# Kernel tuning notes

Measured on AMD Instinct MI355X. Metric: run time of the kernel, lower is better.

## Reference

```python
import jax, jax.numpy as jnp
import numpy as np

N = 50000   # nodes
E = 800000  # edges
F = 64      # node_feature_dim
H = 128     # hidden_dim


def setup_inputs() -> dict:
    key = jax.random.key(0)
    ks = jax.random.split(key, 20)
    def w(k, shape, fan_in):
        return jax.random.normal(k, shape, jnp.float32) / np.sqrt(fan_in)
    return {
        "x": jax.random.normal(ks[0], (N, F), jnp.float32),
        "edge_index": jax.random.randint(ks[1], (2, E), 0, N, jnp.int32),
        "enc_w1": w(ks[2], (F, H), F), "enc_b1": jnp.zeros((H,), jnp.float32),
        "enc_w2": w(ks[3], (H, H), H), "enc_b2": jnp.zeros((H,), jnp.float32),
        "w_c1": w(ks[4], (H, H), H), "b_c1": jnp.zeros((H,), jnp.float32),
        "w_c2": w(ks[5], (H, H), H), "b_c2": jnp.zeros((H,), jnp.float32),
        "w_c3": w(ks[6], (H, H), H), "b_c3": jnp.zeros((H,), jnp.float32),
        "dec_w1": w(ks[7], (H, H), H), "dec_b1": jnp.zeros((H,), jnp.float32),
        "dec_w2": w(ks[8], (H, F), H), "dec_b2": jnp.zeros((F,), jnp.float32),
    }


def _gcn_conv(h, W, b, src, dst, dinv):
    # PyG GCNConv: D^-1/2 (A+I) D^-1/2 (h W) + b  (self-loops already in src/dst)
    hw = h @ W                                   # [N, H]
    norm = dinv[src] * dinv[dst]                 # [E+N]
    msg = hw[src] * norm[:, None]                # gather + scale
    return jax.ops.segment_sum(msg, dst, num_segments=N) + b


def reference(x, edge_index, enc_w1, enc_b1, enc_w2, enc_b2,
              w_c1, b_c1, w_c2, b_c2, w_c3, b_c3,
              dec_w1, dec_b1, dec_w2, dec_b2):
    loop = jnp.arange(N, dtype=edge_index.dtype)
    src = jnp.concatenate([edge_index[0], loop])
    dst = jnp.concatenate([edge_index[1], loop])
    deg = jax.ops.segment_sum(jnp.ones_like(dst, jnp.float32), dst, num_segments=N)
    dinv = jax.lax.rsqrt(deg)  # deg >= 1 because of self-loops

    h = jax.nn.relu(x @ enc_w1 + enc_b1) @ enc_w2 + enc_b2  # encoder MLP
    h = jax.nn.relu(_gcn_conv(h, w_c1, b_c1, src, dst, dinv))
    h = jax.nn.relu(_gcn_conv(h, w_c2, b_c2, src, dst, dinv))
    h = jax.nn.relu(_gcn_conv(h, w_c3, b_c3, src, dst, dinv))
    # window_size == 1: chunk+cat is identity
    out = jax.nn.relu(h @ dec_w1 + dec_b1) @ dec_w2 + dec_b2  # decoder MLP
    return jax.nn.sigmoid(out)
```

## Files before the change

### kernel.cpp

```cpp
#include <hip/hip_runtime.h>
#include <stdint.h>

#define NN 50000
#define NE 800000
#define FD 64
#define HD 128
#define NBKT 196
#define BCAP 5120
#define P1E 4096

static_assert(NN % 16 == 0, "16-row tiles are exact");

typedef __attribute__((ext_vector_type(8))) short short8;
typedef __attribute__((ext_vector_type(4))) float f32x4;

#define AS1 __attribute__((address_space(1)))
#define AS3 __attribute__((address_space(3)))

__device__ __forceinline__ float bflo(unsigned int v) {
    union { unsigned int u; float f; } c; c.u = v << 16; return c.f;
}
__device__ __forceinline__ float bfhi(unsigned int v) {
    union { unsigned int u; float f; } c; c.u = v & 0xffff0000u; return c.f;
}
__device__ __forceinline__ unsigned short f2bf(float f) {
    union { float f; unsigned int u; } c; c.f = f;
    unsigned int u = c.u;
    return (unsigned short)((u + 0x7fffu + ((u >> 16) & 1u)) >> 16);
}
__device__ __forceinline__ unsigned int pack2(float a, float b) {
    return (unsigned int)f2bf(a) | ((unsigned int)f2bf(b) << 16);
}

__device__ __forceinline__ void scan256(int v, int tid, int* __restrict__ out,
                                        int* __restrict__ wsum)
{
    int x = v;
    #pragma unroll
    for (int d = 1; d < 64; d <<= 1) {
        int y = __shfl_up(x, d, 64);
        if ((tid & 63) >= d) x += y;
    }
    if ((tid & 63) == 63) wsum[tid >> 6] = x;
    __syncthreads();
    int add = 0;
    #pragma unroll
    for (int w = 0; w < 4; w++) if (w < (tid >> 6)) add += wsum[w];
    out[tid] = x + add;
    __syncthreads();
}

template <int K, int COLS, int EPI, bool BIAS, bool RSCALE, bool A_F32, bool OUT_F32, bool WCVT>
__device__ __forceinline__ void mgemm_dev(
    int bid,
    const void* __restrict__ Av,
    const void* __restrict__ Wt,
    const float* __restrict__ bias,
    const float* __restrict__ dinv,
    void* __restrict__ outv, int nrows)
{
    constexpr int NB = COLS / 16;
    constexpr int KC = K / 32;
    constexpr int GMASK = (K >> 3) - 1;
    __shared__ __align__(16) unsigned char Ws8[COLS * K * 2];

    const int tid = threadIdx.x;
    const int wave = tid >> 6;
    const int lane = tid & 63;

    if constexpr (WCVT) {
        const float* wf = (const float*)Wt;
        unsigned short* ws = (unsigned short*)Ws8;
        #pragma unroll
        for (int i = 0; i < K * COLS / 256; i++) {
            const int e = i * 256 + tid;
            const int k = e / COLS, c = e % COLS;
            const int gsw = (k >> 3) ^ (c & GMASK);
            ws[c * K + gsw * 8 + (k & 7)] = f2bf(wf[e]);
        }
    } else {
        constexpr int ROUNDS = COLS * K * 2 / 4096;
        const int gb = wave * 1024 + lane * 16;
        const int lb = wave * 1024;
        #pragma unroll
        for (int r = 0; r < ROUNDS; r++) {
            __builtin_amdgcn_global_load_lds(
                (const AS1 unsigned int*)((const unsigned char*)Wt + r * 4096 + gb),
                (AS3 unsigned int*)(Ws8 + r * 4096 + lb),
                16, 0, 0);
        }
    }

    const int m = lane & 15;
    const int q = lane >> 4;
    const int row0 = bid * 64 + wave * 16;

    f32x4 acc[NB];
    #pragma unroll
    for (int i = 0; i < NB; i++) acc[i] = (f32x4){0.f, 0.f, 0.f, 0.f};

    const bool arow_ok = !A_F32 || (row0 + m) < nrows;

    short8 af[KC];
    #pragma unroll
    for (int kc = 0; kc < KC; kc++) {
        if constexpr (A_F32) {
            const float* arowf = (const float*)Av + (size_t)(row0 + m) * K + q * 8 + kc * 32;
            float4 lo = make_float4(0.f, 0.f, 0.f, 0.f), hi = lo;
            if (arow_ok) { lo = *(const float4*)arowf; hi = *(const float4*)(arowf + 4); }
            af[kc][0] = (short)f2bf(lo.x); af[kc][1] = (short)f2bf(lo.y);
            af[kc][2] = (short)f2bf(lo.z); af[kc][3] = (short)f2bf(lo.w);
            af[kc][4] = (short)f2bf(hi.x); af[kc][5] = (short)f2bf(hi.y);
            af[kc][6] = (short)f2bf(hi.z); af[kc][7] = (short)f2bf(hi.w);
        } else {
            const unsigned short* arow = (const unsigned short*)Av + (size_t)(row0 + m) * K + q * 8 + kc * 32;
            af[kc] = *(const short8*)arow;
        }
    }
    __syncthreads();

    #pragma unroll
    for (int kc = 0; kc < KC; kc++) {
        #pragma unroll
        for (int nb = 0; nb < NB; nb++) {
            const int c = nb * 16 + m;
            const int gsw = (kc * 4 + q) ^ (c & GMASK);
            short8 bf = *(const short8*)&Ws8[(c * K + gsw * 8) * 2];
            acc[nb] = __builtin_amdgcn_mfma_f32_16x16x32_bf16(af[kc], bf, acc[nb], 0, 0, 0);
        }
    }

    float bv[NB];
    #pragma unroll
    for (int nb = 0; nb < NB; nb++) bv[nb] = BIAS ? bias[nb * 16 + m] : 0.f;

    #pragma unroll
    for (int r = 0; r < 4; r++) {
        int row = row0 + q * 4 + r;
        if (row < nrows) {
            float sc = RSCALE ? dinv[row] : 1.f;
            #pragma unroll
            for (int nb = 0; nb < NB; nb++) {
                float t = acc[nb][r];
                if (RSCALE) t *= sc;
                t += bv[nb];
                if (EPI == 1) t = fmaxf(t, 0.f);
                if (EPI == 2) t = 1.f / (1.f + __expf(-t));
                if constexpr (OUT_F32) {
                    ((float*)outv)[(size_t)row * COLS + nb * 16 + m] = t;
                } else {
                    ((unsigned short*)outv)[(size_t)row * COLS + nb * 16 + m] = f2bf(t);
                }
            }
        }
    }
}

template <int K, int COLS, int EPI, bool BIAS, bool RSCALE, bool A_F32, bool OUT_F32>
__global__ __launch_bounds__(256) void mgemm_k(
    const void* __restrict__ Av, const unsigned short* __restrict__ Wt,
    const float* __restrict__ bias, const float* __restrict__ dinv,
    void* __restrict__ outv, int nrows)
{
    mgemm_dev<K, COLS, EPI, BIAS, RSCALE, A_F32, OUT_F32, false>(blockIdx.x, Av, Wt, bias, dinv, outv, nrows);
}

__global__ __launch_bounds__(256) void k1_k(
    const float* __restrict__ x, const float* __restrict__ w0,
    const float* __restrict__ enc_b1, unsigned short* __restrict__ bufA,
    const int* __restrict__ src, const int* __restrict__ dst,
    int* __restrict__ gcnt, unsigned int* __restrict__ bucket,
    const float* __restrict__ w1, const float* __restrict__ w2,
    const float* __restrict__ w3, const float* __restrict__ w4,
    const float* __restrict__ w5, const float* __restrict__ w6,
    unsigned short* __restrict__ t1, unsigned short* __restrict__ t2,
    unsigned short* __restrict__ t3, unsigned short* __restrict__ t4,
    unsigned short* __restrict__ t5, unsigned short* __restrict__ t6,
    int gb, int pb)
{
    const int b = blockIdx.x;
    if (b < gb) {
        mgemm_dev<64, 128, 1, true, false, true, false, true>(b, x, w0, enc_b1, nullptr, bufA, NN);
    } else if (b < gb + pb) {
        __shared__ int lcnt[256], lsw[256], lexc[256], lofs[256], lrank[256];
        __shared__ int wsb[4];
        __shared__ unsigned int stage[P1E];
        const int tid = threadIdx.x;
        const int bb = b - gb;
        lcnt[tid] = 0; lrank[tid] = 0;
        __syncthreads();
        unsigned int ent[P1E / 256];
        #pragma unroll
        for (int u = 0; u < P1E / 256; u++) {
            int g = bb * P1E + u * 256 + tid;
            if (g < NE) {
                int d = dst[g], s = src[g];
                int bk = d >> 8;
                atomicAdd(&lcnt[bk], 1);
                ent[u] = (unsigned int)s | ((unsigned int)(d & 255) << 16)
                       | ((unsigned int)bk << 24);
            } else ent[u] = 0xFFFFFFFFu;
        }
        __syncthreads();
        const int v = lcnt[tid];
        scan256(v, tid, lsw, wsb);
        lexc[tid] = lsw[tid] - v;
        lofs[tid] = (v > 0) ? atomicAdd(&gcnt[tid], v) : 0;
        __syncthreads();
        #pragma unroll
        for (int u = 0; u < P1E / 256; u++) {
            if (ent[u] != 0xFFFFFFFFu) {
                int bk = ent[u] >> 24;
                int r = atomicAdd(&lrank[bk], 1);
                stage[lexc[bk] + r] = ent[u];
            }
        }
        __syncthreads();
        int cb = NE - bb * P1E; if (cb > P1E) cb = P1E;
        for (int i = tid; i < cb; i += 256) {
            unsigned int e = stage[i];
            int bk = e >> 24;
            bucket[(size_t)bk * BCAP + lofs[bk] + (i - lexc[bk])] = e;
        }
    } else {
        int b2 = b - gb - pb;
        const float* W; unsigned short* T; int C = 128;
        if      (b2 <  64) { W = w1; T = t1; }
        else if (b2 < 128) { W = w2; T = t2; b2 -= 64; }
        else if (b2 < 192) { W = w3; T = t3; b2 -= 128; }
        else if (b2 < 256) { W = w4; T = t4; b2 -= 192; }
        else if (b2 < 320) { W = w5; T = t5; b2 -= 256; }
        else               { W = w6; T = t6; b2 -= 320; C = 64; }
        int e = b2 * 256 + threadIdx.x;
        int k, c;
        if (C == 128) { k = e >> 7; c = e & 127; } else { k = e >> 6; c = e & 63; }
        int gsw = (k >> 3) ^ (c & 15);
        T[c * 128 + gsw * 8 + (k & 7)] = f2bf(W[e]);
    }
}

__global__ __launch_bounds__(256) void k2_k(
    const unsigned short* __restrict__ bufA, const unsigned short* __restrict__ t1,
    const float* __restrict__ enc_b2, unsigned short* __restrict__ bufB,
    const int* __restrict__ gcnt, const unsigned int* __restrict__ bucket,
    int* __restrict__ off, float* __restrict__ dinv,
    unsigned short* __restrict__ csr, int gb)
{
    if ((int)blockIdx.x < gb) {
        mgemm_dev<128, 128, 0, true, false, false, false, false>(blockIdx.x, bufA, t1, enc_b2, nullptr, bufB, NN);
    } else {
        __shared__ int lc[256], sw[256], sexc[256], lr[256], gsh[256];
        __shared__ int wsb[4];
        const int tid = threadIdx.x;
        const int b = blockIdx.x - gb;
        const int gv = (tid < NBKT) ? gcnt[tid] : 0;
        scan256(gv, tid, gsh, wsb);
        const int cb = gcnt[b];
        const int base = gsh[b] - cb;
        unsigned int ent[BCAP / 256];
        #pragma unroll
        for (int u = 0; u < BCAP / 256; u++) {
            int i = u * 256 + tid;
            ent[u] = (i < cb) ? bucket[(size_t)b * BCAP + i] : 0xFFFFFFFFu;
        }
        lc[tid] = 0; lr[tid] = 0;
        __syncthreads();
        #pragma unroll
        for (int u = 0; u < BCAP / 256; u++)
            if (ent[u] != 0xFFFFFFFFu) atomicAdd(&lc[(ent[u] >> 16) & 255], 1);
        __syncthreads();
        const int v = lc[tid];
        const int node = b * 256 + tid;
        if (node < NN) dinv[node] = rsqrtf((float)(v + 1));
        scan256(v, tid, sw, wsb);
        sexc[tid] = sw[tid] - v;
        if (node < NN) off[node] = base + sexc[tid];
        if (b == NBKT - 1 && tid == 0) off[NN] = NE;
        __syncthreads();
        #pragma unroll
        for (int u = 0; u < BCAP / 256; u++) {
            if (ent[u] != 0xFFFFFFFFu) {
                int dl = (ent[u] >> 16) & 255;
                int r = atomicAdd(&lr[dl], 1);
                csr[base + sexc[dl] + r] = (unsigned short)(ent[u] & 0xffff);
            }
        }
    }
}

__device__ __forceinline__ void gather16_dev(
    const uint4* __restrict__ hws, const int* __restrict__ off,
    const unsigned short* __restrict__ csr, const float* __restrict__ dinv,
    const float* __restrict__ gbias, uint4* __restrict__ g4, int bid, int tid)
{
    const int g = tid >> 4;
    const int l = tid & 15;
    const int row = bid * 16 + g;
    const float4 b0 = *(const float4*)(gbias + 8 * l);
    const float4 b1 = *(const float4*)(gbias + 8 * l + 4);

    uint4 v = hws[(size_t)row * 16 + l];
    float s0 = bflo(v.x), s1 = bfhi(v.x), s2 = bflo(v.y), s3 = bfhi(v.y);
    float s4 = bflo(v.z), s5 = bfhi(v.z), s6 = bflo(v.w), s7 = bfhi(v.w);
    const int je = off[row + 1];
    int j = off[row];
    for (; j + 8 <= je; j += 8) {
        uint4 t[8];
        #pragma unroll
        for (int u = 0; u < 8; u++) t[u] = hws[(size_t)csr[j + u] * 16 + l];
        #pragma unroll
        for (int u = 0; u < 8; u++) {
            s0 += bflo(t[u].x); s1 += bfhi(t[u].x);
            s2 += bflo(t[u].y); s3 += bfhi(t[u].y);
            s4 += bflo(t[u].z); s5 += bfhi(t[u].z);
            s6 += bflo(t[u].w); s7 += bfhi(t[u].w);
        }
    }
    for (; j < je; j++) {
        uint4 t = hws[(size_t)csr[j] * 16 + l];
        s0 += bflo(t.x); s1 += bfhi(t.x);
        s2 += bflo(t.y); s3 += bfhi(t.y);
        s4 += bflo(t.z); s5 += bfhi(t.z);
        s6 += bflo(t.w); s7 += bfhi(t.w);
    }
    const float di = dinv[row];
    uint4 o;
    o.x = pack2(fmaxf(fmaf(di, s0, b0.x), 0.f), fmaxf(fmaf(di, s1, b0.y), 0.f));
    o.y = pack2(fmaxf(fmaf(di, s2, b0.z), 0.f), fmaxf(fmaf(di, s3, b0.w), 0.f));
    o.z = pack2(fmaxf(fmaf(di, s4, b1.x), 0.f), fmaxf(fmaf(di, s5, b1.y), 0.f));
    o.w = pack2(fmaxf(fmaf(di, s6, b1.z), 0.f), fmaxf(fmaf(di, s7, b1.w), 0.f));
    g4[g * 16 + (l ^ g)] = o;
}

template <int EPI, bool BIAS, bool RSCALE>
__global__ __launch_bounds__(256) void aggm16_k(
    const uint4* __restrict__ hws, const int* __restrict__ off,
    const unsigned short* __restrict__ csr, const float* __restrict__ dinv,
    const float* __restrict__ gbias,
    const unsigned short* __restrict__ Wt,
    const float* __restrict__ obias,
    unsigned short* __restrict__ out)
{
    __shared__ __align__(16) uint4 g4[16 * 16];

    const int tid = threadIdx.x;
    const int bid = blockIdx.x;
    const int wave = tid >> 6;
    const int lane = tid & 63;
    const int m = lane & 15;
    const int q = lane >> 4;

    short8 Bf0[4], Bf1[4];
    #pragma unroll
    for (int kc = 0; kc < 4; kc++) {
        const int c0 = wave * 32 + m;
        const int c1 = c0 + 16;
        Bf0[kc] = *(const short8*)&Wt[c0 * 128 + (((kc * 4 + q) ^ (c0 & 15)) << 3)];
        Bf1[kc] = *(const short8*)&Wt[c1 * 128 + (((kc * 4 + q) ^ (c1 & 15)) << 3)];
    }

    gather16_dev(hws, off, csr, dinv, gbias, g4, bid, tid);
    __syncthreads();

    f32x4 a0 = (f32x4){0.f, 0.f, 0.f, 0.f}, a1 = a0;
    #pragma unroll
    for (int kc = 0; kc < 4; kc++) {
        short8 af = *(const short8*)&g4[m * 16 + ((q + kc * 4) ^ m)];
        a0 = __builtin_amdgcn_mfma_f32_16x16x32_bf16(af, Bf0[kc], a0, 0, 0, 0);
        a1 = __builtin_amdgcn_mfma_f32_16x16x32_bf16(af, Bf1[kc], a1, 0, 0, 0);
    }

    const int c0 = wave * 32 + m;
    const int c1 = c0 + 16;
    const float bv0 = BIAS ? obias[c0] : 0.f;
    const float bv1 = BIAS ? obias[c1] : 0.f;

    #pragma unroll
    for (int r = 0; r < 4; r++) {
        const int row = bid * 16 + q * 4 + r;
        const float sc = RSCALE ? dinv[row] : 1.f;
        float t0 = a0[r], t1 = a1[r];
        if (RSCALE) { t0 *= sc; t1 *= sc; }
        t0 += bv0; t1 += bv1;
        if (EPI == 1) { t0 = fmaxf(t0, 0.f); t1 = fmaxf(t1, 0.f); }
        out[(size_t)row * 128 + c0] = f2bf(t0);
        out[(size_t)row * 128 + c1] = f2bf(t1);
    }
}

__global__ __launch_bounds__(256) void decf16_k(
    const uint4* __restrict__ hws, const int* __restrict__ off,
    const unsigned short* __restrict__ csr, const float* __restrict__ dinv,
    const float* __restrict__ gbias,
    const unsigned short* __restrict__ Wt1,
    const float* __restrict__ db1,
    const unsigned short* __restrict__ Wt2,
    const float* __restrict__ db2,
    float* __restrict__ outp)
{
    __shared__ __align__(16) uint4 g4[16 * 16];
    __shared__ __align__(16) uint4 h4[16 * 16];

    const int tid = threadIdx.x;
    const int bid = blockIdx.x;
    const int wave = tid >> 6;
    const int lane = tid & 63;
    const int m = lane & 15;
    const int q = lane >> 4;

    short8 Wf0[4], Wf1[4];
    #pragma unroll
    for (int kc = 0; kc < 4; kc++) {
        const int c0 = wave * 32 + m;
        const int c1 = c0 + 16;
        Wf0[kc] = *(const short8*)&Wt1[c0 * 128 + (((kc * 4 + q) ^ (c0 & 15)) << 3)];
        Wf1[kc] = *(const short8*)&Wt1[c1 * 128 + (((kc * 4 + q) ^ (c1 & 15)) << 3)];
    }

    gather16_dev(hws, off, csr, dinv, gbias, g4, bid, tid);
    __syncthreads();

    f32x4 at0 = (f32x4){0.f, 0.f, 0.f, 0.f}, at1 = at0;
    #pragma unroll
    for (int kc = 0; kc < 4; kc++) {
        short8 gf = *(const short8*)&g4[m * 16 + ((q + kc * 4) ^ m)];
        at0 = __builtin_amdgcn_mfma_f32_16x16x32_bf16(Wf0[kc], gf, at0, 0, 0, 0);
        at1 = __builtin_amdgcn_mfma_f32_16x16x32_bf16(Wf1[kc], gf, at1, 0, 0, 0);
    }

    short8 Bf2[4];
    #pragma unroll
    for (int kc = 0; kc < 4; kc++) {
        const int c = wave * 16 + m;
        Bf2[kc] = *(const short8*)&Wt2[c * 128 + (((kc * 4 + q) ^ (c & 15)) << 3)];
    }

    {
        uint2* h2 = (uint2*)h4;
        {
            const int F = wave * 32 + q * 4;
            const float4 bb = *(const float4*)(db1 + F);
            uint2 hv;
            hv.x = pack2(fmaxf(at0[0] + bb.x, 0.f), fmaxf(at0[1] + bb.y, 0.f));
            hv.y = pack2(fmaxf(at0[2] + bb.z, 0.f), fmaxf(at0[3] + bb.w, 0.f));
            const int cf = wave * 4 + (q >> 1);
            h2[m * 32 + (((cf ^ m) << 1) | (q & 1))] = hv;
        }
        {
            const int F = wave * 32 + 16 + q * 4;
            const float4 bb = *(const float4*)(db1 + F);
            uint2 hv;
            hv.x = pack2(fmaxf(at1[0] + bb.x, 0.f), fmaxf(at1[1] + bb.y, 0.f));
            hv.y = pack2(fmaxf(at1[2] + bb.z, 0.f), fmaxf(at1[3] + bb.w, 0.f));
            const int cf = wave * 4 + 2 + (q >> 1);
            h2[m * 32 + (((cf ^ m) << 1) | (q & 1))] = hv;
        }
    }
    __syncthreads();

    f32x4 a2 = (f32x4){0.f, 0.f, 0.f, 0.f};
    #pragma unroll
    for (int kc = 0; kc < 4; kc++) {
        short8 af = *(const short8*)&h4[m * 16 + ((q + kc * 4) ^ m)];
        a2 = __builtin_amdgcn_mfma_f32_16x16x32_bf16(af, Bf2[kc], a2, 0, 0, 0);
    }

    const int c = wave * 16 + m;
    const float bv = db2[c];
    #pragma unroll
    for (int r = 0; r < 4; r++) {
        const int row = bid * 16 + q * 4 + r;
        float t = a2[r] + bv;
        t = 1.f / (1.f + __expf(-t));
        outp[(size_t)row * 64 + c] = t;
    }
}

extern "C" void kernel_launch(void* const* d_in, const int* in_sizes, int n_in,
                              void* d_out, int out_size, void* d_ws, size_t ws_size,
                              hipStream_t stream)
{
    const float* x      = (const float*)d_in[0];
    const int*   ei     = (const int*)d_in[1];
    const float* enc_w1 = (const float*)d_in[2];
    const float* enc_b1 = (const float*)d_in[3];
    const float* enc_w2 = (const float*)d_in[4];
    const float* enc_b2 = (const float*)d_in[5];
    const float* w_c1   = (const float*)d_in[6];
    const float* b_c1   = (const float*)d_in[7];
    const float* w_c2   = (const float*)d_in[8];
    const float* b_c2   = (const float*)d_in[9];
    const float* w_c3   = (const float*)d_in[10];
    const float* b_c3   = (const float*)d_in[11];
    const float* dec_w1 = (const float*)d_in[12];
    const float* dec_b1 = (const float*)d_in[13];
    const float* dec_w2 = (const float*)d_in[14];
    const float* dec_b2 = (const float*)d_in[15];

    const int* src = ei;
    const int* dst = ei + NE;

    const int NP = 50048;

    char* ws = (char*)d_ws;
    size_t o = 0;
    auto alloc = [&](size_t bytes) -> void* {
        void* p = ws + o;
        o = (o + bytes + 255) & ~(size_t)255;
        return p;
    };
    int*   gcnt = (int*)alloc(256 * 4);
    int*   off  = (int*)alloc((size_t)(NN + 1) * 4);
    unsigned short* csr = (unsigned short*)alloc((size_t)NE * 2);
    unsigned int* bucket = (unsigned int*)alloc((size_t)NBKT * BCAP * 4);
    float* dinv = (float*)alloc((size_t)NN * 4);
    unsigned short* bufA = (unsigned short*)alloc((size_t)NP * HD * 2);
    unsigned short* bufB = (unsigned short*)alloc((size_t)NP * HD * 2);
    unsigned short* t1 = (unsigned short*)alloc(128 * 128 * 2);
    unsigned short* t2 = (unsigned short*)alloc(128 * 128 * 2);
    unsigned short* t3 = (unsigned short*)alloc(128 * 128 * 2);
    unsigned short* t4 = (unsigned short*)alloc(128 * 128 * 2);
    unsigned short* t5 = (unsigned short*)alloc(128 * 128 * 2);
    unsigned short* t6 = (unsigned short*)alloc(128 * 64 * 2);
    (void)ws_size; (void)n_in; (void)in_sizes; (void)out_size;

    hipMemsetAsync(gcnt, 0, 256 * 4, stream);

    const int PB   = (NE + P1E - 1) / P1E;
    const int GB   = NP / 64;
    const int GB16 = NN / 16;

    k1_k<<<GB + PB + 352, 256, 0, stream>>>(x, enc_w1, enc_b1, bufA, src, dst, gcnt, bucket,
                                            enc_w2, w_c1, w_c2, w_c3, dec_w1, dec_w2,
                                            t1, t2, t3, t4, t5, t6, GB, PB);
    k2_k<<<GB + NBKT, 256, 0, stream>>>(bufA, t1, enc_b2, bufB, gcnt, bucket,
                                        off, dinv, csr, GB);
    mgemm_k<128, 128, 0, false, true, false, false><<<GB, 256, 0, stream>>>(bufB, t2, nullptr, dinv, bufA, NN);
    aggm16_k<0, false, true><<<GB16, 256, 0, stream>>>((const uint4*)bufA, off, csr, dinv, b_c1, t3, nullptr, bufB);
    aggm16_k<0, false, true><<<GB16, 256, 0, stream>>>((const uint4*)bufB, off, csr, dinv, b_c2, t4, nullptr, bufA);
    decf16_k<<<GB16, 256, 0, stream>>>((const uint4*)bufA, off, csr, dinv, b_c3,
                                       t5, dec_b1, t6, dec_b2, (float*)d_out);
}
```

Baseline: 263.8 us.

## Split fused gather+GEMM into column-sliced gather and separate GEMM kernels

Replaces the fused aggregate-then-MFMA kernels with a GEMM that writes its output in a column-sliced layout (8 slices of 16 features, node-major within each slice), followed by a gather kernel where each block processes one slice for 128 nodes. The aim is to make the neighbour gather cache-friendlier, since each slice is about 1.6 MB and can stay resident in L2 while being randomly accessed. The cost is extra kernel launches and an extra round trip of the intermediate through global memory between the gather and the GEMM.

```diff
diff --git a/kernel.cpp b/kernel.cpp
--- a/kernel.cpp
+++ b/kernel.cpp
@@ -13,6 +13,7 @@
 
 typedef __attribute__((ext_vector_type(8))) short short8;
 typedef __attribute__((ext_vector_type(4))) float f32x4;
+typedef unsigned int u32x4 __attribute__((ext_vector_type(4)));
 
 #define AS1 __attribute__((address_space(1)))
 #define AS3 __attribute__((address_space(3)))
@@ -50,7 +51,8 @@
     __syncthreads();
 }
 
-template <int K, int COLS, int EPI, bool BIAS, bool RSCALE, bool A_F32, bool OUT_F32, bool WCVT>
+template <int K, int COLS, int EPI, bool BIAS, bool RSCALE, bool A_F32, bool OUT_F32,
+          bool WCVT, bool OUT_SL8>
 __device__ __forceinline__ void mgemm_dev(
     int bid,
     const void* __restrict__ Av,
@@ -148,6 +150,8 @@
                 if (EPI == 2) t = 1.f / (1.f + __expf(-t));
                 if constexpr (OUT_F32) {
                     ((float*)outv)[(size_t)row * COLS + nb * 16 + m] = t;
+                } else if constexpr (OUT_SL8) {
+                    ((unsigned short*)outv)[((size_t)nb * NN + row) * 16 + m] = f2bf(t);
                 } else {
                     ((unsigned short*)outv)[(size_t)row * COLS + nb * 16 + m] = f2bf(t);
                 }
@@ -156,13 +160,14 @@
     }
 }
 
-template <int K, int COLS, int EPI, bool BIAS, bool RSCALE, bool A_F32, bool OUT_F32>
+template <int K, int COLS, int EPI, bool BIAS, bool RSCALE, bool A_F32, bool OUT_F32, bool OUT_SL8>
 __global__ __launch_bounds__(256) void mgemm_k(
     const void* __restrict__ Av, const unsigned short* __restrict__ Wt,
     const float* __restrict__ bias, const float* __restrict__ dinv,
     void* __restrict__ outv, int nrows)
 {
-    mgemm_dev<K, COLS, EPI, BIAS, RSCALE, A_F32, OUT_F32, false>(blockIdx.x, Av, Wt, bias, dinv, outv, nrows);
+    mgemm_dev<K, COLS, EPI, BIAS, RSCALE, A_F32, OUT_F32, false, OUT_SL8>(
+        blockIdx.x, Av, Wt, bias, dinv, outv, nrows);
 }
 
 __global__ __launch_bounds__(256) void k1_k(
@@ -180,7 +185,7 @@
 {
     const int b = blockIdx.x;
     if (b < gb) {
-        mgemm_dev<64, 128, 1, true, false, true, false, true>(b, x, w0, enc_b1, nullptr, bufA, NN);
+        mgemm_dev<64, 128, 1, true, false, true, false, true, false>(b, x, w0, enc_b1, nullptr, bufA, NN);
     } else if (b < gb + pb) {
         __shared__ int lcnt[256], lsw[256], lexc[256], lofs[256], lrank[256];
         __shared__ int wsb[4];
@@ -247,7 +252,8 @@
     unsigned short* __restrict__ csr, int gb)
 {
     if ((int)blockIdx.x < gb) {
-        mgemm_dev<128, 128, 0, true, false, false, false, false>(blockIdx.x, bufA, t1, enc_b2, nullptr, bufB, NN);
+        mgemm_dev<128, 128, 0, true, false, false, false, false, false>(
+            blockIdx.x, bufA, t1, enc_b2, nullptr, bufB, NN);
     } else {
         __shared__ int lc[256], sw[256], sexc[256], lr[256], gsh[256];
         __shared__ int wsb[4];
@@ -288,6 +294,58 @@
     }
 }
 
+__global__ __launch_bounds__(256) void gath8_k(
+    const uint4* __restrict__ hs, const int* __restrict__ off,
+    const unsigned short* __restrict__ csr, const float* __restrict__ dinv,
+    const float* __restrict__ gbias, uint4* __restrict__ gout)
+{
+    const int bid = blockIdx.x;
+    const int s = bid & 7;
+    const int d = bid >> 3;
+    const int tid = threadIdx.x;
+    const int n = tid >> 1;
+    const int h = tid & 1;
+    const int row = d * 128 + n;
+    if (row >= NN) return;
+
+    const uint4* __restrict__ hss = hs + (size_t)s * NN * 2;
+
+    const float4 b0 = *(const float4*)(gbias + s * 16 + h * 8);
+    const float4 b1 = *(const float4*)(gbias + s * 16 + h * 8 + 4);
+    const float di = dinv[row];
+
+    uint4 v = hss[(size_t)row * 2 + h];
+    float s0 = bflo(v.x), s1 = bfhi(v.x), s2 = bflo(v.y), s3 = bfhi(v.y);
+    float s4 = bflo(v.z), s5 = bfhi(v.z), s6 = bflo(v.w), s7 = bfhi(v.w);
+    const int je = off[row + 1];
+    int j = off[row];
+    for (; j + 8 <= je; j += 8) {
+        uint4 t[8];
+        #pragma unroll
+        for (int u = 0; u < 8; u++) t[u] = hss[(size_t)csr[j + u] * 2 + h];
+        #pragma unroll
+        for (int u = 0; u < 8; u++) {
+            s0 += bflo(t[u].x); s1 += bfhi(t[u].x);
+            s2 += bflo(t[u].y); s3 += bfhi(t[u].y);
+            s4 += bflo(t[u].z); s5 += bfhi(t[u].z);
+            s6 += bflo(t[u].w); s7 += bfhi(t[u].w);
+        }
+    }
+    for (; j < je; j++) {
+        uint4 t = hss[(size_t)csr[j] * 2 + h];
+        s0 += bflo(t.x); s1 += bfhi(t.x);
+        s2 += bflo(t.y); s3 += bfhi(t.y);
+        s4 += bflo(t.z); s5 += bfhi(t.z);
+        s6 += bflo(t.w); s7 += bfhi(t.w);
+    }
+    u32x4 o;
+    o[0] = pack2(fmaxf(fmaf(di, s0, b0.x), 0.f), fmaxf(fmaf(di, s1, b0.y), 0.f));
+    o[1] = pack2(fmaxf(fmaf(di, s2, b0.z), 0.f), fmaxf(fmaf(di, s3, b0.w), 0.f));
+    o[2] = pack2(fmaxf(fmaf(di, s4, b1.x), 0.f), fmaxf(fmaf(di, s5, b1.y), 0.f));
+    o[3] = pack2(fmaxf(fmaf(di, s6, b1.z), 0.f), fmaxf(fmaf(di, s7, b1.w), 0.f));
+    __builtin_nontemporal_store(o, (u32x4*)&gout[(size_t)row * 16 + s * 2 + h]);
+}
+
 __device__ __forceinline__ void gather16_dev(
     const uint4* __restrict__ hws, const int* __restrict__ off,
     const unsigned short* __restrict__ csr, const float* __restrict__ dinv,
@@ -330,62 +388,6 @@
     o.z = pack2(fmaxf(fmaf(di, s4, b1.x), 0.f), fmaxf(fmaf(di, s5, b1.y), 0.f));
     o.w = pack2(fmaxf(fmaf(di, s6, b1.z), 0.f), fmaxf(fmaf(di, s7, b1.w), 0.f));
     g4[g * 16 + (l ^ g)] = o;
-}
-
-template <int EPI, bool BIAS, bool RSCALE>
-__global__ __launch_bounds__(256) void aggm16_k(
-    const uint4* __restrict__ hws, const int* __restrict__ off,
-    const unsigned short* __restrict__ csr, const float* __restrict__ dinv,
-    const float* __restrict__ gbias,
-    const unsigned short* __restrict__ Wt,
-    const float* __restrict__ obias,
-    unsigned short* __restrict__ out)
-{
-    __shared__ __align__(16) uint4 g4[16 * 16];
-
-    const int tid = threadIdx.x;
-    const int bid = blockIdx.x;
-    const int wave = tid >> 6;
-    const int lane = tid & 63;
-    const int m = lane & 15;
-    const int q = lane >> 4;
-
-    short8 Bf0[4], Bf1[4];
-    #pragma unroll
-    for (int kc = 0; kc < 4; kc++) {
-        const int c0 = wave * 32 + m;
-        const int c1 = c0 + 16;
-        Bf0[kc] = *(const short8*)&Wt[c0 * 128 + (((kc * 4 + q) ^ (c0 & 15)) << 3)];
-        Bf1[kc] = *(const short8*)&Wt[c1 * 128 + (((kc * 4 + q) ^ (c1 & 15)) << 3)];
-    }
-
-    gather16_dev(hws, off, csr, dinv, gbias, g4, bid, tid);
-    __syncthreads();
-
-    f32x4 a0 = (f32x4){0.f, 0.f, 0.f, 0.f}, a1 = a0;
-    #pragma unroll
-    for (int kc = 0; kc < 4; kc++) {
-        short8 af = *(const short8*)&g4[m * 16 + ((q + kc * 4) ^ m)];
-        a0 = __builtin_amdgcn_mfma_f32_16x16x32_bf16(af, Bf0[kc], a0, 0, 0, 0);
-        a1 = __builtin_amdgcn_mfma_f32_16x16x32_bf16(af, Bf1[kc], a1, 0, 0, 0);
-    }
-
-    const int c0 = wave * 32 + m;
-    const int c1 = c0 + 16;
-    const float bv0 = BIAS ? obias[c0] : 0.f;
-    const float bv1 = BIAS ? obias[c1] : 0.f;
-
-    #pragma unroll
-    for (int r = 0; r < 4; r++) {
-        const int row = bid * 16 + q * 4 + r;
-        const float sc = RSCALE ? dinv[row] : 1.f;
-        float t0 = a0[r], t1 = a1[r];
-        if (RSCALE) { t0 *= sc; t1 *= sc; }
-        t0 += bv0; t1 += bv1;
-        if (EPI == 1) { t0 = fmaxf(t0, 0.f); t1 = fmaxf(t1, 0.f); }
-        out[(size_t)row * 128 + c0] = f2bf(t0);
-        out[(size_t)row * 128 + c1] = f2bf(t1);
-    }
 }
 
 __global__ __launch_bounds__(256) void decf16_k(
@@ -529,15 +531,21 @@
     const int PB   = (NE + P1E - 1) / P1E;
     const int GB   = NP / 64;
     const int GB16 = NN / 16;
+    const int G8   = 8 * ((NN + 127) / 128);
 
     k1_k<<<GB + PB + 352, 256, 0, stream>>>(x, enc_w1, enc_b1, bufA, src, dst, gcnt, bucket,
                                             enc_w2, w_c1, w_c2, w_c3, dec_w1, dec_w2,
                                             t1, t2, t3, t4, t5, t6, GB, PB);
     k2_k<<<GB + NBKT, 256, 0, stream>>>(bufA, t1, enc_b2, bufB, gcnt, bucket,
                                         off, dinv, csr, GB);
-    mgemm_k<128, 128, 0, false, true, false, false><<<GB, 256, 0, stream>>>(bufB, t2, nullptr, dinv, bufA, NN);
-    aggm16_k<0, false, true><<<GB16, 256, 0, stream>>>((const uint4*)bufA, off, csr, dinv, b_c1, t3, nullptr, bufB);
-    aggm16_k<0, false, true><<<GB16, 256, 0, stream>>>((const uint4*)bufB, off, csr, dinv, b_c2, t4, nullptr, bufA);
+    mgemm_k<128, 128, 0, false, true, false, false, true><<<GB, 256, 0, stream>>>(
+        bufB, t2, nullptr, dinv, bufA, NN);
+    gath8_k<<<G8, 256, 0, stream>>>((const uint4*)bufA, off, csr, dinv, b_c1, (uint4*)bufB);
+    mgemm_k<128, 128, 0, false, true, false, false, true><<<GB, 256, 0, stream>>>(
+        bufB, t3, nullptr, dinv, bufA, NN);
+    gath8_k<<<G8, 256, 0, stream>>>((const uint4*)bufA, off, csr, dinv, b_c2, (uint4*)bufB);
+    mgemm_k<128, 128, 0, false, true, false, false, false><<<GB, 256, 0, stream>>>(
+        bufB, t4, nullptr, dinv, bufA, NN);
     decf16_k<<<GB16, 256, 0, stream>>>((const uint4*)bufA, off, csr, dinv, b_c3,
                                        t5, dec_b1, t6, dec_b2, (float*)d_out);
 }
```

New measurement: 279.2 us. 1.06x slower.
